# Performance work log

Hardware: AMD Instinct MI355X
Metric: run time of the kernel (lower is better)

Reference implementation:

```python
import jax, jax.numpy as jnp
import numpy as np

OUT_H, OUT_W = 64, 64  # glimpse size (layer's output_dim)
B, IMG_H, IMG_W, CH = 32, 512, 512, 3


def setup_inputs() -> dict:
    key = jax.random.key(0)
    k_img, k_u, k_s, k_d, k_u2, k_s2, k_d2 = jax.random.split(key, 7)
    img_tensor = jax.random.uniform(k_img, (B, IMG_H, IMG_W, CH), dtype=jnp.float32)
    # DRAW-style params per sample: (uy, sy, dy, ux, sx, dx)
    # centres u in [0, img - glimpse], sigma s in [1, 5], stride d in [1, img/glimpse]
    uy = jax.random.uniform(k_u, (B, 1), minval=0.0, maxval=IMG_H - OUT_H * 2.0)
    sy = jax.random.uniform(k_s, (B, 1), minval=1.0, maxval=5.0)
    dy = jax.random.uniform(k_d, (B, 1), minval=1.0, maxval=IMG_H / OUT_H)
    ux = jax.random.uniform(k_u2, (B, 1), minval=0.0, maxval=IMG_W - OUT_W * 2.0)
    sx = jax.random.uniform(k_s2, (B, 1), minval=1.0, maxval=5.0)
    dx = jax.random.uniform(k_d2, (B, 1), minval=1.0, maxval=IMG_W / OUT_W)
    transform_params = jnp.concatenate([uy, sy, dy, ux, sx, dx], axis=-1)  # (B, 6)
    return {"img_tensor": img_tensor, "transform_params": transform_params}


def gaussian_mask(u, s, d, R, C):
    """Normalized Gaussian filterbank.
    u, s, d: (B, 1) centre of first Gaussian, std, stride between centres.
    R: number of glimpse rows/cols; C: image size along that axis.
    Returns (B, C, R), each column normalized to sum 1 (plus eps)."""
    r = jnp.arange(R, dtype=jnp.float32).reshape(1, 1, R)
    c = jnp.arange(C, dtype=jnp.float32).reshape(1, C, 1)
    centres = u[:, None, :] + r * d[:, None, :]            # (B, 1, R)
    mask = jnp.exp(-0.5 * jnp.square((c - centres) / s[:, None, :]))  # (B, C, R)
    return mask / (jnp.sum(mask, axis=1, keepdims=True) + 1e-8)


def reference(img_tensor, transform_params):
    # img_tensor: (B, h, w, ch); transform_params: (B, 6)
    _, h, w, _ = img_tensor.shape
    uy, sy, dy, ux, sx, dx = jnp.split(transform_params, 6, axis=-1)
    Ay = gaussian_mask(uy, sy, dy, OUT_H, h)  # (B, h, OUT_H)
    Ax = gaussian_mask(ux, sx, dx, OUT_W, w)  # (B, w, OUT_W)
    # glimpse = Ay^T @ img @ Ax, applied per channel
    g = jnp.einsum('bhH,bhwc->bHwc', Ay, img_tensor)   # (B, OUT_H, w, ch)
    return jnp.einsum('bHwc,bwW->bHWc', g, Ax)         # (B, OUT_H, OUT_W, ch)
```

## Files before the change

kernel.cpp:

```cpp
#include <hip/hip_runtime.h>
#include <stdint.h>

#define BATCH 32
#define IMG 512
#define CH 3
#define GOUT 64
#define ROWB (IMG*CH)
#define GP   ((size_t)BATCH*CH*GOUT*IMG)

typedef __attribute__((ext_vector_type(8))) short  short8;
typedef __attribute__((ext_vector_type(4))) float  floatx4;

__device__ __forceinline__ unsigned short f2bf(float x) {
    unsigned u = __builtin_bit_cast(unsigned, x);
    u += 0x7FFFu + ((u >> 16) & 1u);
    return (unsigned short)(u >> 16);
}

typedef __attribute__((address_space(3))) unsigned int  lds_u32;
typedef __attribute__((address_space(1))) const unsigned int g_u32;
__device__ __forceinline__ void async16(const void* g, void* l) {
    __builtin_amdgcn_global_load_lds((g_u32*)(uintptr_t)g,
                                     (lds_u32*)(uintptr_t)l, 16, 0, 0);
}

__global__ __launch_bounds__(64) void mask_kernel(const float* __restrict__ tp,
                                                  unsigned short* __restrict__ AyT,
                                                  unsigned short* __restrict__ AxT) {
    int blk  = blockIdx.x;
    int r    = blk & 63;
    int axis = (blk >> 6) & 1;
    int b    = blk >> 7;

    const float* p = tp + b*6 + (axis ? 3 : 0);
    float u = p[0], s = p[1], d = p[2];
    float centre = u + (float)r * d;
    float inv_s  = 1.0f / s;

    int lane = threadIdx.x;
    float e[8];
    float sum = 0.0f;
    #pragma unroll
    for (int i = 0; i < 8; ++i) {
        float z = ((float)(i*64 + lane) - centre) * inv_s;
        e[i] = __expf(-0.5f * z * z);
        sum += e[i];
    }
    #pragma unroll
    for (int m = 1; m < 64; m <<= 1)
        sum += __shfl_xor(sum, m, 64);
    float inv_sum = 1.0f / (sum + 1e-8f);

    unsigned short* dst = (axis ? AxT : AyT) + ((size_t)b*GOUT + r) * IMG;
    #pragma unroll
    for (int i = 0; i < 8; ++i)
        dst[i*64 + lane] = f2bf(e[i] * inv_sum);
}

__global__ __launch_bounds__(256, 6) void stage1_kernel(const float* __restrict__ img,
                                                        const unsigned short* __restrict__ AyT,
                                                        float* __restrict__ gP) {
    __shared__ float          Bs[64][64];
    __shared__ unsigned short As[64][72];

    int part = blockIdx.x & 1;
    int bt   = blockIdx.x >> 1;
    int tile = bt % 24;
    int b    = bt / 24;
    int wc0  = tile * 64;
    int tid  = threadIdx.x;
    int wave = tid >> 6;
    int lane = tid & 63;
    int n16  = lane & 15;
    int q    = lane >> 4;

    floatx4 acc[4];
    #pragma unroll
    for (int mt = 0; mt < 4; ++mt) acc[mt] = (floatx4){0.f, 0.f, 0.f, 0.f};

    const float*          imb = img + (size_t)b * IMG * ROWB + wc0;
    const unsigned short* ayb = AyT + (size_t)b * GOUT * IMG;

    int rb = (tid >> 6)*4 + ((tid & 63) >> 4);
    int cg = tid & 15;

    for (int h0 = part*256; h0 < part*256 + 256; h0 += 64) {
        uint4 av[2];
        #pragma unroll
        for (int i = 0; i < 2; ++i) {
            int p = tid + i*256;
            av[i] = *(const uint4*)(ayb + (size_t)(p >> 3) * IMG + h0 + (p & 7)*8);
        }
        #pragma unroll
        for (int i = 0; i < 4; ++i) {
            int r = rb + i*16;
            async16(imb + (size_t)(h0 + r) * ROWB + cg*4, &Bs[r][cg*4]);
        }
        #pragma unroll
        for (int i = 0; i < 2; ++i) {
            int p = tid + i*256;
            *(uint4*)&As[p >> 3][(p & 7)*8] = av[i];
        }
        __syncthreads();

        #pragma unroll
        for (int s = 0; s < 2; ++s) {
            short8 bf;
            #pragma unroll
            for (int j = 0; j < 8; ++j)
                bf[j] = (short)f2bf(Bs[s*32 + q*8 + j][wave*16 + n16]);
            #pragma unroll
            for (int mt = 0; mt < 4; ++mt) {
                short8 af = *(const short8*)&As[mt*16 + n16][s*32 + q*8];
                acc[mt] = __builtin_amdgcn_mfma_f32_16x16x32_bf16(af, bf, acc[mt], 0, 0, 0);
            }
        }
        __syncthreads();
    }

    int wc = wc0 + wave*16 + n16;
    int c = wc % 3, w = wc / 3;
    float* gb = gP + (size_t)part * GP + ((size_t)(b*CH + c) * GOUT) * IMG + w;
    #pragma unroll
    for (int mt = 0; mt < 4; ++mt)
        #pragma unroll
        for (int reg = 0; reg < 4; ++reg)
            gb[(size_t)(mt*16 + q*4 + reg) * IMG] = acc[mt][reg];
}

__global__ __launch_bounds__(256) void stage2_kernel(const float* __restrict__ gP,
                                                     const unsigned short* __restrict__ AxT,
                                                     float* __restrict__ out) {
    int blk  = blockIdx.x;
    int part = blk & 3;
    int bc   = blk >> 2;
    int c    = bc % 3;
    int b    = bc / 3;
    int tid  = threadIdx.x;
    int wm   = tid >> 6;
    int lane = tid & 63;
    int n16  = lane & 15;
    int q    = lane >> 4;

    floatx4 acc[4];
    #pragma unroll
    for (int nt = 0; nt < 4; ++nt) acc[nt] = (floatx4){0.f, 0.f, 0.f, 0.f};

    const float*          ga  = gP  + ((size_t)(b*CH + c) * GOUT + wm*16 + n16) * IMG;
    const unsigned short* axb = AxT + ((size_t)b*GOUT + n16) * IMG;

    #pragma unroll
    for (int cc = 0; cc < 4; ++cc) {
        int w0 = part*128 + cc*32;
        const float* ap = ga + w0 + q*8;
        float4 a0 = *(const float4*)ap;
        float4 a1 = *(const float4*)(ap + 4);
        float4 b0 = *(const float4*)(ap + GP);
        float4 b1 = *(const float4*)(ap + GP + 4);
        short8 af;
        af[0] = (short)f2bf(a0.x + b0.x); af[1] = (short)f2bf(a0.y + b0.y);
        af[2] = (short)f2bf(a0.z + b0.z); af[3] = (short)f2bf(a0.w + b0.w);
        af[4] = (short)f2bf(a1.x + b1.x); af[5] = (short)f2bf(a1.y + b1.y);
        af[6] = (short)f2bf(a1.z + b1.z); af[7] = (short)f2bf(a1.w + b1.w);

        #pragma unroll
        for (int nt = 0; nt < 4; ++nt) {
            short8 bf = *(const short8*)(axb + (size_t)nt*16*IMG + w0 + q*8);
            acc[nt] = __builtin_amdgcn_mfma_f32_16x16x32_bf16(af, bf, acc[nt], 0, 0, 0);
        }
    }

    #pragma unroll
    for (int nt = 0; nt < 4; ++nt) {
        int W = nt*16 + n16;
        #pragma unroll
        for (int reg = 0; reg < 4; ++reg) {
            int H = wm*16 + q*4 + reg;
            atomicAdd(out + (((size_t)b*GOUT + H) * GOUT + W) * CH + c, acc[nt][reg]);
        }
    }
}

extern "C" void kernel_launch(void* const* d_in, const int* in_sizes, int n_in,
                              void* d_out, int out_size, void* d_ws, size_t ws_size,
                              hipStream_t stream) {
    const float* img = (const float*)d_in[0];
    const float* tp  = (const float*)d_in[1];
    float* out = (float*)d_out;

    unsigned short* AyT = (unsigned short*)d_ws;
    unsigned short* AxT = AyT + (size_t)BATCH * GOUT * IMG;
    float*          gPp = (float*)(AxT + (size_t)BATCH * GOUT * IMG);

    hipMemsetAsync(d_out, 0, (size_t)out_size * sizeof(float), stream);
    mask_kernel  <<<BATCH * 2 * GOUT,   64, 0, stream>>>(tp, AyT, AxT);
    stage1_kernel<<<BATCH * 24 * 2,    256, 0, stream>>>(img, AyT, gPp);
    stage2_kernel<<<BATCH * CH * 4,    256, 0, stream>>>(gPp, AxT, out);
}
```

Measured before the change: 186.3 us.

## Drop LDS staging in stage1 and split stage2 by output rows without atomics

Stage1 no longer stages image and Ay tiles through shared memory with async copies and barriers. Each lane now loads its image column and Ay fragment directly from global memory, so the __syncthreads calls go away and occupancy is freed from LDS limits. In exchange, the image reads become strided per-lane scalar loads. Stage2 now gives each block a 16-row slice of output H and the full W reduction, so it writes results directly instead of using atomicAdd, which also removes the output memset.

```diff
diff --git a/kernel.cpp b/kernel.cpp
--- a/kernel.cpp
+++ b/kernel.cpp
@@ -15,13 +15,6 @@
     unsigned u = __builtin_bit_cast(unsigned, x);
     u += 0x7FFFu + ((u >> 16) & 1u);
     return (unsigned short)(u >> 16);
-}
-
-typedef __attribute__((address_space(3))) unsigned int  lds_u32;
-typedef __attribute__((address_space(1))) const unsigned int g_u32;
-__device__ __forceinline__ void async16(const void* g, void* l) {
-    __builtin_amdgcn_global_load_lds((g_u32*)(uintptr_t)g,
-                                     (lds_u32*)(uintptr_t)l, 16, 0, 0);
 }
 
 __global__ __launch_bounds__(64) void mask_kernel(const float* __restrict__ tp,
@@ -57,12 +50,9 @@
         dst[i*64 + lane] = f2bf(e[i] * inv_sum);
 }
 
-__global__ __launch_bounds__(256, 6) void stage1_kernel(const float* __restrict__ img,
+__global__ __launch_bounds__(256, 4) void stage1_kernel(const float* __restrict__ img,
                                                         const unsigned short* __restrict__ AyT,
                                                         float* __restrict__ gP) {
-    __shared__ float          Bs[64][64];
-    __shared__ unsigned short As[64][72];
-
     int part = blockIdx.x & 1;
     int bt   = blockIdx.x >> 1;
     int tile = bt % 24;
@@ -78,44 +68,21 @@
     #pragma unroll
     for (int mt = 0; mt < 4; ++mt) acc[mt] = (floatx4){0.f, 0.f, 0.f, 0.f};
 
-    const float*          imb = img + (size_t)b * IMG * ROWB + wc0;
+    const float*          imb = img + (size_t)b * IMG * ROWB + wc0 + wave*16 + n16;
     const unsigned short* ayb = AyT + (size_t)b * GOUT * IMG;
 
-    int rb = (tid >> 6)*4 + ((tid & 63) >> 4);
-    int cg = tid & 15;
-
-    for (int h0 = part*256; h0 < part*256 + 256; h0 += 64) {
-        uint4 av[2];
+    for (int h0 = part*256; h0 < part*256 + 256; h0 += 32) {
+        int hk = h0 + q*8;
+        const float* ip = imb + (size_t)hk * ROWB;
+        short8 bf;
         #pragma unroll
-        for (int i = 0; i < 2; ++i) {
-            int p = tid + i*256;
-            av[i] = *(const uint4*)(ayb + (size_t)(p >> 3) * IMG + h0 + (p & 7)*8);
+        for (int j = 0; j < 8; ++j)
+            bf[j] = (short)f2bf(ip[(size_t)j * ROWB]);
+        #pragma unroll
+        for (int mt = 0; mt < 4; ++mt) {
+            short8 af = *(const short8*)(ayb + (size_t)(mt*16 + n16) * IMG + hk);
+            acc[mt] = __builtin_amdgcn_mfma_f32_16x16x32_bf16(af, bf, acc[mt], 0, 0, 0);
         }
-        #pragma unroll
-        for (int i = 0; i < 4; ++i) {
-            int r = rb + i*16;
-            async16(imb + (size_t)(h0 + r) * ROWB + cg*4, &Bs[r][cg*4]);
-        }
-        #pragma unroll
-        for (int i = 0; i < 2; ++i) {
-            int p = tid + i*256;
-            *(uint4*)&As[p >> 3][(p & 7)*8] = av[i];
-        }
-        __syncthreads();
-
-        #pragma unroll
-        for (int s = 0; s < 2; ++s) {
-            short8 bf;
-            #pragma unroll
-            for (int j = 0; j < 8; ++j)
-                bf[j] = (short)f2bf(Bs[s*32 + q*8 + j][wave*16 + n16]);
-            #pragma unroll
-            for (int mt = 0; mt < 4; ++mt) {
-                short8 af = *(const short8*)&As[mt*16 + n16][s*32 + q*8];
-                acc[mt] = __builtin_amdgcn_mfma_f32_16x16x32_bf16(af, bf, acc[mt], 0, 0, 0);
-            }
-        }
-        __syncthreads();
     }
 
     int wc = wc0 + wave*16 + n16;
@@ -132,53 +99,42 @@
                                                      const unsigned short* __restrict__ AxT,
                                                      float* __restrict__ out) {
     int blk  = blockIdx.x;
-    int part = blk & 3;
+    int hq   = blk & 3;
     int bc   = blk >> 2;
     int c    = bc % 3;
     int b    = bc / 3;
     int tid  = threadIdx.x;
-    int wm   = tid >> 6;
+    int wave = tid >> 6;
     int lane = tid & 63;
     int n16  = lane & 15;
     int q    = lane >> 4;
 
-    floatx4 acc[4];
-    #pragma unroll
-    for (int nt = 0; nt < 4; ++nt) acc[nt] = (floatx4){0.f, 0.f, 0.f, 0.f};
+    floatx4 acc = (floatx4){0.f, 0.f, 0.f, 0.f};
 
-    const float*          ga  = gP  + ((size_t)(b*CH + c) * GOUT + wm*16 + n16) * IMG;
-    const unsigned short* axb = AxT + ((size_t)b*GOUT + n16) * IMG;
+    const float*          ga  = gP  + ((size_t)(b*CH + c) * GOUT + hq*16 + n16) * IMG;
+    const unsigned short* axb = AxT + ((size_t)b*GOUT + wave*16 + n16) * IMG;
 
-    #pragma unroll
-    for (int cc = 0; cc < 4; ++cc) {
-        int w0 = part*128 + cc*32;
-        const float* ap = ga + w0 + q*8;
-        float4 a0 = *(const float4*)ap;
-        float4 a1 = *(const float4*)(ap + 4);
-        float4 b0 = *(const float4*)(ap + GP);
-        float4 b1 = *(const float4*)(ap + GP + 4);
+    #pragma unroll 4
+    for (int cc = 0; cc < 16; ++cc) {
+        int w0 = cc*32 + q*8;
+        float4 a0 = *(const float4*)(ga + w0);
+        float4 a1 = *(const float4*)(ga + w0 + 4);
+        float4 b0 = *(const float4*)(ga + GP + w0);
+        float4 b1 = *(const float4*)(ga + GP + w0 + 4);
         short8 af;
         af[0] = (short)f2bf(a0.x + b0.x); af[1] = (short)f2bf(a0.y + b0.y);
         af[2] = (short)f2bf(a0.z + b0.z); af[3] = (short)f2bf(a0.w + b0.w);
         af[4] = (short)f2bf(a1.x + b1.x); af[5] = (short)f2bf(a1.y + b1.y);
         af[6] = (short)f2bf(a1.z + b1.z); af[7] = (short)f2bf(a1.w + b1.w);
 
-        #pragma unroll
-        for (int nt = 0; nt < 4; ++nt) {
-            short8 bf = *(const short8*)(axb + (size_t)nt*16*IMG + w0 + q*8);
-            acc[nt] = __builtin_amdgcn_mfma_f32_16x16x32_bf16(af, bf, acc[nt], 0, 0, 0);
-        }
+        short8 bf = *(const short8*)(axb + w0);
+        acc = __builtin_amdgcn_mfma_f32_16x16x32_bf16(af, bf, acc, 0, 0, 0);
     }
 
+    float* ob = out + (((size_t)b*GOUT + hq*16) * GOUT + wave*16 + n16) * CH + c;
     #pragma unroll
-    for (int nt = 0; nt < 4; ++nt) {
-        int W = nt*16 + n16;
-        #pragma unroll
-        for (int reg = 0; reg < 4; ++reg) {
-            int H = wm*16 + q*4 + reg;
-            atomicAdd(out + (((size_t)b*GOUT + H) * GOUT + W) * CH + c, acc[nt][reg]);
-        }
-    }
+    for (int reg = 0; reg < 4; ++reg)
+        ob[(size_t)(q*4 + reg) * GOUT * CH] = acc[reg];
 }
 
 extern "C" void kernel_launch(void* const* d_in, const int* in_sizes, int n_in,
@@ -192,8 +148,7 @@
     unsigned short* AxT = AyT + (size_t)BATCH * GOUT * IMG;
     float*          gPp = (float*)(AxT + (size_t)BATCH * GOUT * IMG);
 
-    hipMemsetAsync(d_out, 0, (size_t)out_size * sizeof(float), stream);
-    mask_kernel  <<<BATCH * 2 * GOUT,   64, 0, stream>>>(tp, AyT, AxT);
-    stage1_kernel<<<BATCH * 24 * 2,    256, 0, stream>>>(img, AyT, gPp);
-    stage2_kernel<<<BATCH * CH * 4,    256, 0, stream>>>(gPp, AxT, out);
+    mask_kernel  <<<BATCH * 2 * GOUT,  64, 0, stream>>>(tp, AyT, AxT);
+    stage1_kernel<<<BATCH * 24 * 2,   256, 0, stream>>>(img, AyT, gPp);
+    stage2_kernel<<<BATCH * CH * 4,   256, 0, stream>>>(gPp, AxT, out);
 }
```

Result: slower. 200.2 us (+7.4%).
